# Optimization experiments

Hardware: AMD Instinct MI355X
Metric: run time of the kernel (lower is better)

## Reference

```python
import jax, jax.numpy as jnp
import numpy as np

N, E = 50000, 800000          # nodes, edges
IN, HID, H, OUT = 128, 64, 4, 64  # in_size, hid_size, num_heads, out_size
NEG_SLOPE = 0.2               # DGL GATConv default leaky_relu slope
EPS = 1e-5                    # LayerNorm eps


def setup_inputs() -> dict:
    key = jax.random.key(0)
    ks = jax.random.split(key, 20)
    f32 = jnp.float32

    def nrm(k, shape, fan_in):
        return jax.random.normal(k, shape, f32) * (1.0 / np.sqrt(fan_in))

    inp = {}
    inp['feats'] = jax.random.normal(ks[0], (N, IN), f32)
    inp['src'] = jax.random.randint(ks[1], (E,), 0, N, jnp.int32)
    inp['dst'] = jnp.sort(jax.random.randint(ks[2], (E,), 0, N, jnp.int32))
    # GATConv 0: in -> H*HID, bias=False
    inp['W0'] = nrm(ks[3], (IN, H * HID), IN)
    inp['al0'] = nrm(ks[4], (H, HID), HID)
    inp['ar0'] = nrm(ks[5], (H, HID), HID)
    # residual linear 0
    inp['resw0'] = nrm(ks[6], (IN, HID), IN)
    inp['resb0'] = jnp.zeros((HID,), f32)
    # LayerNorm 0
    inp['g0'] = jnp.ones((HID,), f32)
    inp['b0'] = jnp.zeros((HID,), f32)
    # GATConv 1: hid -> H*HID (out_linear=True so last layer is hid->hid)
    inp['W1'] = nrm(ks[7], (HID, H * HID), HID)
    inp['al1'] = nrm(ks[8], (H, HID), HID)
    inp['ar1'] = nrm(ks[9], (H, HID), HID)
    # residual linear 1
    inp['resw1'] = nrm(ks[10], (HID, HID), HID)
    inp['resb1'] = jnp.zeros((HID,), f32)
    # LayerNorm 1
    inp['g1'] = jnp.ones((HID,), f32)
    inp['b1'] = jnp.zeros((HID,), f32)
    # final prediction head
    inp['predw'] = nrm(ks[11], (HID, OUT), HID)
    inp['predb'] = jnp.zeros((OUT,), f32)
    return inp


def _gat_conv(h, W, al, ar, src, dst):
    """DGL GATConv (bias=False, no internal residual), returns [N,H,Dh]."""
    Hh, Dh = al.shape
    fs = (h @ W).reshape(-1, Hh, Dh)              # [N,H,Dh]
    el = jnp.einsum('nhd,hd->nh', fs, al)         # [N,H]
    er = jnp.einsum('nhd,hd->nh', fs, ar)
    e = jax.nn.leaky_relu(el[src] + er[dst], NEG_SLOPE)  # [E,H]
    # edge softmax over incoming edges of each destination node
    emax = jax.ops.segment_max(e, dst, num_segments=N, indices_are_sorted=True)
    a = jnp.exp(e - emax[dst])
    asum = jax.ops.segment_sum(a, dst, num_segments=N, indices_are_sorted=True)
    a = a / asum[dst]
    msg = a[:, :, None] * fs[src]                 # [E,H,Dh]
    return jax.ops.segment_sum(msg, dst, num_segments=N, indices_are_sorted=True)


def _layer_norm(x, g, b):
    mu = jnp.mean(x, axis=-1, keepdims=True)
    var = jnp.mean(jnp.square(x - mu), axis=-1, keepdims=True)
    return (x - mu) / jnp.sqrt(var + EPS) * g + b


def reference(feats, src, dst, W0, al0, ar0, resw0, resb0, g0, b0,
              W1, al1, ar1, resw1, resb1, g1, b1, predw, predb):
    # layer 0: conv.mean(heads) + residual linear, then LN + ReLU (dropout=0)
    h = _gat_conv(feats, W0, al0, ar0, src, dst).mean(axis=1) + (feats @ resw0 + resb0)
    h = jax.nn.relu(_layer_norm(h, g0, b0))
    # layer 1 (out_linear=True -> same treatment)
    h = _gat_conv(h, W1, al1, ar1, src, dst).mean(axis=1) + (h @ resw1 + resb1)
    h = jax.nn.relu(_layer_norm(h, g1, b1))
    # final prediction
    return h @ predw + predb
```

## Files before the change

kernel.cpp:

```cpp
#include <hip/hip_runtime.h>
#include <hip/hip_bf16.h>

#define N_NODES 50000
#define E_EDGES 800000
#define NH 4
#define NEG_SLOPE 0.2f
#define LN_EPS 1e-5f

typedef short short8v __attribute__((ext_vector_type(8)));
typedef float f32x4  __attribute__((ext_vector_type(4)));

__device__ __forceinline__ unsigned short f2bf(float x) {
    __hip_bfloat16 h = __float2bfloat16(x);
    unsigned short u;
    __builtin_memcpy(&u, &h, sizeof(u));
    return u;
}

__global__ void k_rowptr(const int* __restrict__ dst, int* __restrict__ rp) {
    int d = blockIdx.x * blockDim.x + threadIdx.x;
    if (d > N_NODES) return;
    int lo = 0, hi = E_EDGES;
    while (lo < hi) {
        int mid = (lo + hi) >> 1;
        if (dst[mid] < d) lo = mid + 1; else hi = mid;
    }
    rp[d] = lo;
}

__global__ void k_wprep(const float* __restrict__ W0, const float* __restrict__ rw0,
                        short* __restrict__ Vt0,
                        const float* __restrict__ W1, const float* __restrict__ rw1,
                        short* __restrict__ Vt1)
{
    int idx = blockIdx.x * 256 + threadIdx.x;
    if (idx < 320 * 128) {
        int c = idx >> 7, k = idx & 127;
        float v = (c < 256) ? W0[k * 256 + c] : rw0[k * 64 + (c - 256)];
        Vt0[c * 128 + k] = (short)f2bf(v);
    }
    int i1 = idx - 320 * 128;
    if (i1 >= 0 && i1 < 320 * 64) {
        int c = i1 >> 6, k = i1 & 63;
        float v = (c < 256) ? W1[k * 256 + c] : rw1[k * 64 + (c - 256)];
        Vt1[c * 64 + k] = (short)f2bf(v);
    }
}

__global__ void k_hprep(const float* __restrict__ hin, unsigned int* __restrict__ hb) {
    const long long i8 = (long long)(blockIdx.x * 256 + threadIdx.x) * 8;
    if (i8 >= (long long)N_NODES * 128) return;
    const float4 a = *(const float4*)(hin + i8);
    const float4 b = *(const float4*)(hin + i8 + 4);
    uint4 pk;
    pk.x = (unsigned)f2bf(a.x) | ((unsigned)f2bf(a.y) << 16);
    pk.y = (unsigned)f2bf(a.z) | ((unsigned)f2bf(a.w) << 16);
    pk.z = (unsigned)f2bf(b.x) | ((unsigned)f2bf(b.y) << 16);
    pk.w = (unsigned)f2bf(b.z) | ((unsigned)f2bf(b.w) << 16);
    *(uint4*)(hb + (i8 >> 1)) = pk;
}

template<int K>
__global__ __launch_bounds__(256) void k_gemm(
    const short* __restrict__ hb, const short* __restrict__ Vt,
    const float* __restrict__ al, const float* __restrict__ ar,
    const float* __restrict__ resb,
    __hip_bfloat16* __restrict__ fs, float* __restrict__ el,
    float* __restrict__ er, float* __restrict__ resid)
{
    const int n0  = blockIdx.x * 16;
    const int t   = threadIdx.x;
    const int w   = t >> 6;
    const int l   = t & 63;
    const int c16 = l & 15;
    const int ks  = l >> 4;

    constexpr int NKB = K / 32;
    f32x4 acc[5];
    #pragma unroll
    for (int i = 0; i < 5; ++i) acc[i] = (f32x4){0.f, 0.f, 0.f, 0.f};

    #pragma unroll
    for (int kb = 0; kb < NKB; ++kb) {
        const int kbase = kb * 32 + ks * 8;
        const short8v af = *(const short8v*)(hb + (size_t)(n0 + c16) * K + kbase);
        #pragma unroll
        for (int i = 0; i < 4; ++i) {
            const int cg = 64 * w + 16 * i + c16;
            short8v bf = *(const short8v*)(Vt + (size_t)cg * K + kbase);
            acc[i] = __builtin_amdgcn_mfma_f32_16x16x32_bf16(af, bf, acc[i], 0, 0, 0);
        }
        {
            const int cg = 256 + 16 * w + c16;
            short8v bf = *(const short8v*)(Vt + (size_t)cg * K + kbase);
            acc[4] = __builtin_amdgcn_mfma_f32_16x16x32_bf16(af, bf, acc[4], 0, 0, 0);
        }
    }

    float el_p[4] = {0.f, 0.f, 0.f, 0.f};
    float er_p[4] = {0.f, 0.f, 0.f, 0.f};
    #pragma unroll
    for (int i = 0; i < 4; ++i) {
        const int cg = 64 * w + 16 * i + c16;
        const float alv = al[cg], arv = ar[cg];
        #pragma unroll
        for (int reg = 0; reg < 4; ++reg) {
            const float v = acc[i][reg];
            const int node = n0 + ks * 4 + reg;
            fs[(size_t)node * 256 + cg] = __float2bfloat16(v);
            el_p[reg] = fmaf(v, alv, el_p[reg]);
            er_p[reg] = fmaf(v, arv, er_p[reg]);
        }
    }
    #pragma unroll
    for (int o = 1; o < 16; o <<= 1) {
        #pragma unroll
        for (int reg = 0; reg < 4; ++reg) {
            el_p[reg] += __shfl_xor(el_p[reg], o, 64);
            er_p[reg] += __shfl_xor(er_p[reg], o, 64);
        }
    }
    if (c16 == 0) {
        #pragma unroll
        for (int reg = 0; reg < 4; ++reg) {
            const int node = n0 + ks * 4 + reg;
            el[node * NH + w] = el_p[reg];
            er[node * NH + w] = er_p[reg];
        }
    }
    {
        const int rc = 16 * w + c16;
        const float bb = resb[rc];
        #pragma unroll
        for (int reg = 0; reg < 4; ++reg) {
            const int node = n0 + ks * 4 + reg;
            resid[(size_t)node * 64 + rc] = acc[4][reg] + bb;
        }
    }
}

template<bool FINAL>
__global__ __launch_bounds__(256) void k_agg(
    const int* __restrict__ rp, const int* __restrict__ src,
    const unsigned int* __restrict__ fs_u,
    const float* __restrict__ el, const float* __restrict__ er,
    const float* __restrict__ resid,
    const float* __restrict__ g, const float* __restrict__ b,
    const float* __restrict__ predw, const float* __restrict__ predb,
    void* __restrict__ outv)
{
    __shared__ __align__(16) float aw[4][64][4];
    __shared__ int   sjw[4][64];
    __shared__ float ylds[4][64];

    const int t    = threadIdx.x;
    const int wv   = t >> 6;
    const int lane = t & 63;
    const int d    = blockIdx.x * 4 + wv;
    const int l    = lane & 31;
    const int h2   = lane >> 5;
    const int hh   = l >> 3;

    const int start = rp[d], end = rp[d + 1];
    const float4 er4 = *(const float4*)(er + (size_t)d * NH);

    float4 s4 = make_float4(0.f, 0.f, 0.f, 0.f);
    float acc[8];
    #pragma unroll
    for (int i = 0; i < 8; ++i) acc[i] = 0.f;

    for (int cs = start; cs < end; cs += 64) {
        const int cnt = min(64, end - cs);
        int   sj = 0;
        float4 a4 = make_float4(0.f, 0.f, 0.f, 0.f);
        if (lane < cnt) {
            sj = src[cs + lane];
            const float4 el4 = *(const float4*)(el + (size_t)sj * NH);
            float ex = el4.x + er4.x; ex = ex > 0.f ? ex : NEG_SLOPE * ex;
            float ey = el4.y + er4.y; ey = ey > 0.f ? ey : NEG_SLOPE * ey;
            float ez = el4.z + er4.z; ez = ez > 0.f ? ez : NEG_SLOPE * ez;
            float ew = el4.w + er4.w; ew = ew > 0.f ? ew : NEG_SLOPE * ew;
            a4.x = __expf(ex); a4.y = __expf(ey);
            a4.z = __expf(ez); a4.w = __expf(ew);
            s4.x += a4.x; s4.y += a4.y; s4.z += a4.z; s4.w += a4.w;
        }
        sjw[wv][lane] = sj;
        *(float4*)&aw[wv][lane][0] = a4;
        #pragma unroll 4
        for (int jj = 0; jj < cnt; jj += 2) {
            const int j2 = jj + h2;
            if (j2 < cnt) {
                const float w = aw[wv][j2][hh];
                const int   s = sjw[wv][j2];
                const uint4 u = *((const uint4*)(fs_u + (size_t)s * 128) + l);
                acc[0] = fmaf(w, __uint_as_float(u.x << 16),         acc[0]);
                acc[1] = fmaf(w, __uint_as_float(u.x & 0xffff0000u), acc[1]);
                acc[2] = fmaf(w, __uint_as_float(u.y << 16),         acc[2]);
                acc[3] = fmaf(w, __uint_as_float(u.y & 0xffff0000u), acc[3]);
                acc[4] = fmaf(w, __uint_as_float(u.z << 16),         acc[4]);
                acc[5] = fmaf(w, __uint_as_float(u.z & 0xffff0000u), acc[5]);
                acc[6] = fmaf(w, __uint_as_float(u.w << 16),         acc[6]);
                acc[7] = fmaf(w, __uint_as_float(u.w & 0xffff0000u), acc[7]);
            }
        }
    }

    #pragma unroll
    for (int i = 0; i < 8; ++i) acc[i] += __shfl_xor(acc[i], 32);

    #pragma unroll
    for (int o = 32; o > 0; o >>= 1) {
        s4.x += __shfl_xor(s4.x, o);
        s4.y += __shfl_xor(s4.y, o);
        s4.z += __shfl_xor(s4.z, o);
        s4.w += __shfl_xor(s4.w, o);
    }
    const float rsx = s4.x > 0.f ? 1.f / s4.x : 0.f;
    const float rsy = s4.y > 0.f ? 1.f / s4.y : 0.f;
    const float rsz = s4.z > 0.f ? 1.f / s4.z : 0.f;
    const float rsw = s4.w > 0.f ? 1.f / s4.w : 0.f;
    const float rsh = hh == 0 ? rsx : hh == 1 ? rsy : hh == 2 ? rsz : rsw;
    #pragma unroll
    for (int i = 0; i < 8; ++i) acc[i] *= rsh;

    #pragma unroll
    for (int i = 0; i < 8; ++i) {
        acc[i] += __shfl_xor(acc[i], 8);
        acc[i] += __shfl_xor(acc[i], 16);
    }

    const int c0 = 8 * (l & 7);
    const float4 r0 = *(const float4*)(resid + (size_t)d * 64 + c0);
    const float4 r1 = *(const float4*)(resid + (size_t)d * 64 + c0 + 4);
    float v[8];
    v[0] = 0.25f * acc[0] + r0.x;  v[1] = 0.25f * acc[1] + r0.y;
    v[2] = 0.25f * acc[2] + r0.z;  v[3] = 0.25f * acc[3] + r0.w;
    v[4] = 0.25f * acc[4] + r1.x;  v[5] = 0.25f * acc[5] + r1.y;
    v[6] = 0.25f * acc[6] + r1.z;  v[7] = 0.25f * acc[7] + r1.w;

    float p = 0.f, p2 = 0.f;
    #pragma unroll
    for (int i = 0; i < 8; ++i) { p += v[i]; p2 += v[i] * v[i]; }
    #pragma unroll
    for (int o = 4; o > 0; o >>= 1) {
        p  += __shfl_xor(p,  o);
        p2 += __shfl_xor(p2, o);
    }
    const float mu  = p * (1.f / 64.f);
    const float var = p2 * (1.f / 64.f) - mu * mu;
    const float inv = 1.f / sqrtf(fmaxf(var, 0.f) + LN_EPS);

    const float4 g0v = *(const float4*)(g + c0);
    const float4 g1v = *(const float4*)(g + c0 + 4);
    const float4 b0v = *(const float4*)(b + c0);
    const float4 b1v = *(const float4*)(b + c0 + 4);
    float y[8];
    y[0] = fmaxf((v[0] - mu) * inv * g0v.x + b0v.x, 0.f);
    y[1] = fmaxf((v[1] - mu) * inv * g0v.y + b0v.y, 0.f);
    y[2] = fmaxf((v[2] - mu) * inv * g0v.z + b0v.z, 0.f);
    y[3] = fmaxf((v[3] - mu) * inv * g0v.w + b0v.w, 0.f);
    y[4] = fmaxf((v[4] - mu) * inv * g1v.x + b1v.x, 0.f);
    y[5] = fmaxf((v[5] - mu) * inv * g1v.y + b1v.y, 0.f);
    y[6] = fmaxf((v[6] - mu) * inv * g1v.z + b1v.z, 0.f);
    y[7] = fmaxf((v[7] - mu) * inv * g1v.w + b1v.w, 0.f);

    if (!FINAL) {
        if (lane < 8) {
            unsigned int* hb1 = (unsigned int*)outv;
            uint4 pk;
            pk.x = (unsigned)f2bf(y[0]) | ((unsigned)f2bf(y[1]) << 16);
            pk.y = (unsigned)f2bf(y[2]) | ((unsigned)f2bf(y[3]) << 16);
            pk.z = (unsigned)f2bf(y[4]) | ((unsigned)f2bf(y[5]) << 16);
            pk.w = (unsigned)f2bf(y[6]) | ((unsigned)f2bf(y[7]) << 16);
            *(uint4*)(hb1 + (size_t)d * 32 + 4 * lane) = pk;
        }
    } else {
        float* out = (float*)outv;
        if (lane < 8) {
            #pragma unroll
            for (int i = 0; i < 8; ++i) ylds[wv][8 * lane + i] = y[i];
        }
        float o = predb[lane];
        #pragma unroll 4
        for (int k = 0; k < 64; ++k)
            o = fmaf(ylds[wv][k], predw[k * 64 + lane], o);
        out[(size_t)d * 64 + lane] = o;
    }
}

extern "C" void kernel_launch(void* const* d_in, const int* in_sizes, int n_in,
                              void* d_out, int out_size, void* d_ws, size_t ws_size,
                              hipStream_t stream)
{
    const float* feats = (const float*)d_in[0];
    const int*   src   = (const int*)  d_in[1];
    const int*   dst   = (const int*)  d_in[2];
    const float* W0    = (const float*)d_in[3];
    const float* al0   = (const float*)d_in[4];
    const float* ar0   = (const float*)d_in[5];
    const float* resw0 = (const float*)d_in[6];
    const float* resb0 = (const float*)d_in[7];
    const float* g0    = (const float*)d_in[8];
    const float* b0    = (const float*)d_in[9];
    const float* W1    = (const float*)d_in[10];
    const float* al1   = (const float*)d_in[11];
    const float* ar1   = (const float*)d_in[12];
    const float* resw1 = (const float*)d_in[13];
    const float* resb1 = (const float*)d_in[14];
    const float* g1    = (const float*)d_in[15];
    const float* b1    = (const float*)d_in[16];
    const float* predw = (const float*)d_in[17];
    const float* predb = (const float*)d_in[18];
    float* out = (float*)d_out;

    char* ws = (char*)d_ws;
    int*   rp = (int*)ws;
    __hip_bfloat16* fs = (__hip_bfloat16*)(ws + 200192);
    float* el    = (float*)((char*)fs + (size_t)N_NODES * 256 * 2);
    float* er    = el + (size_t)N_NODES * 4;
    float* resid = er + (size_t)N_NODES * 4;
    short* hb0   = (short*)(resid + (size_t)N_NODES * 64);
    short* hb1   = hb0 + (size_t)N_NODES * 128;
    short* Vt0   = hb1 + (size_t)N_NODES * 64;
    short* Vt1   = Vt0 + 320 * 128;

    k_rowptr<<<(N_NODES + 1 + 255) / 256, 256, 0, stream>>>(dst, rp);
    k_wprep<<<(320 * 128 + 320 * 64 + 255) / 256, 256, 0, stream>>>(
        W0, resw0, Vt0, W1, resw1, Vt1);
    k_hprep<<<(N_NODES * 128 / 8 + 255) / 256, 256, 0, stream>>>(
        feats, (unsigned int*)hb0);

    k_gemm<128><<<N_NODES / 16, 256, 0, stream>>>(
        hb0, Vt0, al0, ar0, resb0, fs, el, er, resid);
    k_agg<false><<<N_NODES / 4, 256, 0, stream>>>(
        rp, src, (const unsigned int*)fs, el, er, resid, g0, b0,
        nullptr, nullptr, hb1);

    k_gemm<64><<<N_NODES / 16, 256, 0, stream>>>(
        hb1, Vt1, al1, ar1, resb1, fs, el, er, resid);
    k_agg<true><<<N_NODES / 4, 256, 0, stream>>>(
        rp, src, (const unsigned int*)fs, el, er, resid, g1, b1,
        predw, predb, out);
}
```

Measured before the change: 338.1 us.

## Fuse feature bf16 conversion into GEMM, merge prep kernels, double GEMM node tile

Merges the row-pointer binary search and weight transpose/convert into a single prep kernel, and removes the separate fp32-to-bf16 feature conversion kernel by converting feats in registers inside the first GEMM. Each GEMM block now processes 32 nodes with two accumulator sets, reusing each weight fragment load for two MFMAs, with clamping and guarded stores for the tail. This cuts two kernel launches and an intermediate bf16 buffer round trip, at the cost of more registers and extra fp32 load traffic in the first GEMM.

```diff
diff --git a/kernel.cpp b/kernel.cpp
--- a/kernel.cpp
+++ b/kernel.cpp
@@ -17,58 +17,42 @@
     return u;
 }
 
-__global__ void k_rowptr(const int* __restrict__ dst, int* __restrict__ rp) {
-    int d = blockIdx.x * blockDim.x + threadIdx.x;
-    if (d > N_NODES) return;
-    int lo = 0, hi = E_EDGES;
-    while (lo < hi) {
-        int mid = (lo + hi) >> 1;
-        if (dst[mid] < d) lo = mid + 1; else hi = mid;
-    }
-    rp[d] = lo;
-}
-
-__global__ void k_wprep(const float* __restrict__ W0, const float* __restrict__ rw0,
-                        short* __restrict__ Vt0,
-                        const float* __restrict__ W1, const float* __restrict__ rw1,
-                        short* __restrict__ Vt1)
+__global__ void k_prep(const int* __restrict__ dst, int* __restrict__ rp,
+                       const float* __restrict__ W0, const float* __restrict__ rw0,
+                       short* __restrict__ Vt0,
+                       const float* __restrict__ W1, const float* __restrict__ rw1,
+                       short* __restrict__ Vt1)
 {
-    int idx = blockIdx.x * 256 + threadIdx.x;
+    const int idx = blockIdx.x * 256 + threadIdx.x;
+    if (idx <= N_NODES) {
+        int lo = 0, hi = E_EDGES;
+        while (lo < hi) {
+            int mid = (lo + hi) >> 1;
+            if (dst[mid] < idx) lo = mid + 1; else hi = mid;
+        }
+        rp[idx] = lo;
+    }
     if (idx < 320 * 128) {
         int c = idx >> 7, k = idx & 127;
         float v = (c < 256) ? W0[k * 256 + c] : rw0[k * 64 + (c - 256)];
         Vt0[c * 128 + k] = (short)f2bf(v);
-    }
-    int i1 = idx - 320 * 128;
-    if (i1 >= 0 && i1 < 320 * 64) {
+    } else if (idx < 320 * 128 + 320 * 64) {
+        int i1 = idx - 320 * 128;
         int c = i1 >> 6, k = i1 & 63;
         float v = (c < 256) ? W1[k * 256 + c] : rw1[k * 64 + (c - 256)];
         Vt1[c * 64 + k] = (short)f2bf(v);
     }
 }
 
-__global__ void k_hprep(const float* __restrict__ hin, unsigned int* __restrict__ hb) {
-    const long long i8 = (long long)(blockIdx.x * 256 + threadIdx.x) * 8;
-    if (i8 >= (long long)N_NODES * 128) return;
-    const float4 a = *(const float4*)(hin + i8);
-    const float4 b = *(const float4*)(hin + i8 + 4);
-    uint4 pk;
-    pk.x = (unsigned)f2bf(a.x) | ((unsigned)f2bf(a.y) << 16);
-    pk.y = (unsigned)f2bf(a.z) | ((unsigned)f2bf(a.w) << 16);
-    pk.z = (unsigned)f2bf(b.x) | ((unsigned)f2bf(b.y) << 16);
-    pk.w = (unsigned)f2bf(b.z) | ((unsigned)f2bf(b.w) << 16);
-    *(uint4*)(hb + (i8 >> 1)) = pk;
-}
-
-template<int K>
+template<int K, bool AF32>
 __global__ __launch_bounds__(256) void k_gemm(
-    const short* __restrict__ hb, const short* __restrict__ Vt,
+    const void* __restrict__ hA, const short* __restrict__ Vt,
     const float* __restrict__ al, const float* __restrict__ ar,
     const float* __restrict__ resb,
     __hip_bfloat16* __restrict__ fs, float* __restrict__ el,
     float* __restrict__ er, float* __restrict__ resid)
 {
-    const int n0  = blockIdx.x * 16;
+    const int n0  = blockIdx.x * 32;
     const int t   = threadIdx.x;
     const int w   = t >> 6;
     const int l   = t & 63;
@@ -76,65 +60,86 @@
     const int ks  = l >> 4;
 
     constexpr int NKB = K / 32;
-    f32x4 acc[5];
-    #pragma unroll
-    for (int i = 0; i < 5; ++i) acc[i] = (f32x4){0.f, 0.f, 0.f, 0.f};
+    f32x4 acc[2][5];
+    #pragma unroll
+    for (int a = 0; a < 2; ++a)
+        #pragma unroll
+        for (int i = 0; i < 5; ++i) acc[a][i] = (f32x4){0.f, 0.f, 0.f, 0.f};
 
     #pragma unroll
     for (int kb = 0; kb < NKB; ++kb) {
         const int kbase = kb * 32 + ks * 8;
-        const short8v af = *(const short8v*)(hb + (size_t)(n0 + c16) * K + kbase);
+        short8v af[2];
+        #pragma unroll
+        for (int a = 0; a < 2; ++a) {
+            const int rowc = min(n0 + 16 * a + c16, N_NODES - 1);
+            if (AF32) {
+                const float* hf = (const float*)hA;
+                const float4 x = *(const float4*)(hf + (size_t)rowc * K + kbase);
+                const float4 y = *(const float4*)(hf + (size_t)rowc * K + kbase + 4);
+                af[a][0] = (short)f2bf(x.x); af[a][1] = (short)f2bf(x.y);
+                af[a][2] = (short)f2bf(x.z); af[a][3] = (short)f2bf(x.w);
+                af[a][4] = (short)f2bf(y.x); af[a][5] = (short)f2bf(y.y);
+                af[a][6] = (short)f2bf(y.z); af[a][7] = (short)f2bf(y.w);
+            } else {
+                const short* hs = (const short*)hA;
+                af[a] = *(const short8v*)(hs + (size_t)rowc * K + kbase);
+            }
+        }
+        #pragma unroll
+        for (int i = 0; i < 5; ++i) {
+            const int cg = (i < 4) ? (64 * w + 16 * i + c16) : (256 + 16 * w + c16);
+            const short8v bf = *(const short8v*)(Vt + (size_t)cg * K + kbase);
+            acc[0][i] = __builtin_amdgcn_mfma_f32_16x16x32_bf16(af[0], bf, acc[0][i], 0, 0, 0);
+            acc[1][i] = __builtin_amdgcn_mfma_f32_16x16x32_bf16(af[1], bf, acc[1][i], 0, 0, 0);
+        }
+    }
+
+    #pragma unroll
+    for (int a = 0; a < 2; ++a) {
+        float el_p[4] = {0.f, 0.f, 0.f, 0.f};
+        float er_p[4] = {0.f, 0.f, 0.f, 0.f};
         #pragma unroll
         for (int i = 0; i < 4; ++i) {
             const int cg = 64 * w + 16 * i + c16;
-            short8v bf = *(const short8v*)(Vt + (size_t)cg * K + kbase);
-            acc[i] = __builtin_amdgcn_mfma_f32_16x16x32_bf16(af, bf, acc[i], 0, 0, 0);
+            const float alv = al[cg], arv = ar[cg];
+            #pragma unroll
+            for (int reg = 0; reg < 4; ++reg) {
+                const float v = acc[a][i][reg];
+                const int node = n0 + 16 * a + ks * 4 + reg;
+                if (node < N_NODES)
+                    fs[(size_t)node * 256 + cg] = __float2bfloat16(v);
+                el_p[reg] = fmaf(v, alv, el_p[reg]);
+                er_p[reg] = fmaf(v, arv, er_p[reg]);
+            }
+        }
+        #pragma unroll
+        for (int o = 1; o < 16; o <<= 1) {
+            #pragma unroll
+            for (int reg = 0; reg < 4; ++reg) {
+                el_p[reg] += __shfl_xor(el_p[reg], o, 64);
+                er_p[reg] += __shfl_xor(er_p[reg], o, 64);
+            }
+        }
+        if (c16 == 0) {
+            #pragma unroll
+            for (int reg = 0; reg < 4; ++reg) {
+                const int node = n0 + 16 * a + ks * 4 + reg;
+                if (node < N_NODES) {
+                    el[node * NH + w] = el_p[reg];
+                    er[node * NH + w] = er_p[reg];
+                }
+            }
         }
         {
-            const int cg = 256 + 16 * w + c16;
-            short8v bf = *(const short8v*)(Vt + (size_t)cg * K + kbase);
-            acc[4] = __builtin_amdgcn_mfma_f32_16x16x32_bf16(af, bf, acc[4], 0, 0, 0);
-        }
-    }
-
-    float el_p[4] = {0.f, 0.f, 0.f, 0.f};
-    float er_p[4] = {0.f, 0.f, 0.f, 0.f};
-    #pragma unroll
-    for (int i = 0; i < 4; ++i) {
-        const int cg = 64 * w + 16 * i + c16;
-        const float alv = al[cg], arv = ar[cg];
-        #pragma unroll
-        for (int reg = 0; reg < 4; ++reg) {
-            const float v = acc[i][reg];
-            const int node = n0 + ks * 4 + reg;
-            fs[(size_t)node * 256 + cg] = __float2bfloat16(v);
-            el_p[reg] = fmaf(v, alv, el_p[reg]);
-            er_p[reg] = fmaf(v, arv, er_p[reg]);
-        }
-    }
-    #pragma unroll
-    for (int o = 1; o < 16; o <<= 1) {
-        #pragma unroll
-        for (int reg = 0; reg < 4; ++reg) {
-            el_p[reg] += __shfl_xor(el_p[reg], o, 64);
-            er_p[reg] += __shfl_xor(er_p[reg], o, 64);
-        }
-    }
-    if (c16 == 0) {
-        #pragma unroll
-        for (int reg = 0; reg < 4; ++reg) {
-            const int node = n0 + ks * 4 + reg;
-            el[node * NH + w] = el_p[reg];
-            er[node * NH + w] = er_p[reg];
-        }
-    }
-    {
-        const int rc = 16 * w + c16;
-        const float bb = resb[rc];
-        #pragma unroll
-        for (int reg = 0; reg < 4; ++reg) {
-            const int node = n0 + ks * 4 + reg;
-            resid[(size_t)node * 64 + rc] = acc[4][reg] + bb;
+            const int rc = 16 * w + c16;
+            const float bb = resb[rc];
+            #pragma unroll
+            for (int reg = 0; reg < 4; ++reg) {
+                const int node = n0 + 16 * a + ks * 4 + reg;
+                if (node < N_NODES)
+                    resid[(size_t)node * 64 + rc] = acc[a][4][reg] + bb;
+            }
         }
     }
 }
@@ -319,24 +324,19 @@
     float* el    = (float*)((char*)fs + (size_t)N_NODES * 256 * 2);
     float* er    = el + (size_t)N_NODES * 4;
     float* resid = er + (size_t)N_NODES * 4;
-    short* hb0   = (short*)(resid + (size_t)N_NODES * 64);
-    short* hb1   = hb0 + (size_t)N_NODES * 128;
+    short* hb1   = (short*)(resid + (size_t)N_NODES * 64);
     short* Vt0   = hb1 + (size_t)N_NODES * 64;
     short* Vt1   = Vt0 + 320 * 128;
 
-    k_rowptr<<<(N_NODES + 1 + 255) / 256, 256, 0, stream>>>(dst, rp);
-    k_wprep<<<(320 * 128 + 320 * 64 + 255) / 256, 256, 0, stream>>>(
-        W0, resw0, Vt0, W1, resw1, Vt1);
-    k_hprep<<<(N_NODES * 128 / 8 + 255) / 256, 256, 0, stream>>>(
-        feats, (unsigned int*)hb0);
-
-    k_gemm<128><<<N_NODES / 16, 256, 0, stream>>>(
-        hb0, Vt0, al0, ar0, resb0, fs, el, er, resid);
+    k_prep<<<240, 256, 0, stream>>>(dst, rp, W0, resw0, Vt0, W1, resw1, Vt1);
+
+    k_gemm<128, true><<<(N_NODES + 31) / 32, 256, 0, stream>>>(
+        feats, Vt0, al0, ar0, resb0, fs, el, er, resid);
     k_agg<false><<<N_NODES / 4, 256, 0, stream>>>(
         rp, src, (const unsigned int*)fs, el, er, resid, g0, b0,
         nullptr, nullptr, hb1);
 
-    k_gemm<64><<<N_NODES / 16, 256, 0, stream>>>(
+    k_gemm<64, false><<<(N_NODES + 31) / 32, 256, 0, stream>>>(
         hb1, Vt1, al1, ar1, resb1, fs, el, er, resid);
     k_agg<true><<<N_NODES / 4, 256, 0, stream>>>(
         rp, src, (const unsigned int*)fs, el, er, resid, g1, b1,
```

Result: faster. 322.1 us (-4.7%).
